# Kernel optimization log

Measured on AMD Instinct MI355X. Metric: run time of the kernel, lower is better.

Reference implementation:

```python
import jax, jax.numpy as jnp
import numpy as np

N_WIN = 8      # windows per side (j = i = n_win)
NUM_HEADS = 8
TOPK = 4


def setup_inputs() -> dict:
    key = jax.random.key(0)
    k1, k2 = jax.random.split(key)
    cv_feature = jax.random.normal(k1, (1, 128, 128, 256), dtype=jnp.float32)
    mv_feature = jax.random.normal(k2, (1, 4, 128, 128, 256), dtype=jnp.float32)
    return {"cv_feature": cv_feature, "mv_feature": mv_feature}


def reference(cv_feature, mv_feature):
    n, H, W, C = cv_feature.shape
    v = mv_feature.shape[1]
    j = i = N_WIN
    h, w = H // j, W // i
    p2, w2 = j * i, h * w
    m = NUM_HEADS
    ch = C // m
    scale = C ** (-0.5)  # module uses d_model**-0.5 for both routing and pixel attn

    # window partition: n (j h)(i w) c -> n (j i) h w c
    cv_patch = cv_feature.reshape(n, j, h, i, w, C).transpose(0, 1, 3, 2, 4, 5).reshape(n, p2, h, w, C)
    mv_patch = mv_feature.reshape(n, v, j, h, i, w, C).transpose(0, 1, 2, 4, 3, 5, 6).reshape(n, v, p2, h, w, C)

    q_pix = cv_patch.reshape(n, p2, w2, C)          # n p2 w2 c
    kv_pix = mv_patch.reshape(n, v, p2, w2, C)      # n v p2 w2 c

    # window-level pooled queries/keys (routing is detached in the original)
    q_win = jax.lax.stop_gradient(cv_patch.mean((2, 3)))            # n p2 c
    k_win = jax.lax.stop_gradient(mv_patch.mean((3, 4)))            # n v p2 c
    k_win = k_win.reshape(n, v * p2, C)

    logits = jnp.einsum('npc,nqc->npq', q_win * scale, k_win)       # n p2 (v p2)
    topk_logit, r_idx = jax.lax.top_k(logits, TOPK)                 # n p2 k
    r_weight = jax.nn.softmax(topk_logit, axis=-1)                  # computed, unused (faithful)

    # gather routed KV windows: n p2 k w2 c
    kv_flat = kv_pix.reshape(n, v * p2, w2, C)
    kv_sel = jnp.take_along_axis(kv_flat[:, None], r_idx[:, :, :, None, None], axis=2)

    # split heads
    k_sel = kv_sel.reshape(n, p2, TOPK, w2, m, ch)                  # n p2 k w2 m ch
    q = q_pix.reshape(n, p2, w2, m, ch)                             # n p2 w2 m ch

    attn = jnp.einsum('npqmc,npkwmc->npmqkw', q * scale, k_sel)
    attn = attn.reshape(n, p2, m, w2, TOPK * w2)
    attn = jax.nn.softmax(attn, axis=-1)

    v_sel = k_sel.transpose(0, 1, 4, 2, 3, 5).reshape(n, p2, m, TOPK * w2, ch)
    out = jnp.einsum('npmqt,npmtc->npmqc', attn, v_sel)             # n p2 m w2 ch

    # merge heads + window un-partition: -> n H W C
    out = out.transpose(0, 1, 3, 2, 4).reshape(n, j, i, h, w, C)
    out = out.transpose(0, 1, 3, 2, 4, 5).reshape(n, H, W, C)
    return out
```

## Files before the change

### kernel.cpp

```cpp
#include <hip/hip_runtime.h>
#include <hip/hip_bf16.h>


typedef __attribute__((ext_vector_type(4))) float f32x4;
typedef __attribute__((ext_vector_type(8))) short s16x8;
typedef __attribute__((ext_vector_type(2))) unsigned u32x2;
typedef __attribute__((ext_vector_type(4))) unsigned u32x4;

#define SCALE 0.0625f
#define LOG2E 1.44269504088896340736f

__device__ inline unsigned cvt_pk_bf16(float lo, float hi) {
  unsigned r;
  asm("v_cvt_pk_bf16_f32 %0, %1, %2" : "=v"(r) : "v"(lo), "v"(hi));
  return r;
}
__device__ inline unsigned pk_bf16_rne(float lo, float hi) {
  unsigned a = __float_as_uint(lo);
  unsigned b = __float_as_uint(hi);
  a += 0x7FFFu + ((a >> 16) & 1u);
  b += 0x7FFFu + ((b >> 16) & 1u);
  return (a >> 16) | (b & 0xFFFF0000u);
}
#if __has_builtin(__builtin_amdgcn_exp2f)
#define EXP2(x) __builtin_amdgcn_exp2f(x)
#else
#define EXP2(x) exp2f(x)
#endif

__global__ __launch_bounds__(256) void k_means(const float* __restrict__ cv,
                                               const float* __restrict__ mv,
                                               float* __restrict__ qwin,
                                               float* __restrict__ kwin) {
  __shared__ f32x4 sm[8][32];
  int wi = blockIdx.x >> 1, half = blockIdx.x & 1;
  int c4 = threadIdx.x & 31, pq = threadIdx.x >> 5;
  const float* base;
  float* dst;
  if (wi < 64) {
    base = cv + ((size_t)((wi >> 3) * 16) * 128 + (wi & 7) * 16) * 256;
    dst = qwin + wi * 256;
  } else {
    int r = wi - 64;
    base = mv + (size_t)(r >> 6) * (128 * 128 * 256)
         + ((size_t)(((r >> 3) & 7) * 16) * 128 + (r & 7) * 16) * 256;
    dst = kwin + r * 256;
  }
  base += half * 128 + c4 * 4;
  f32x4 acc = {0.f, 0.f, 0.f, 0.f};
#pragma unroll 4
  for (int k = 0; k < 32; ++k) {
    int px = pq * 32 + k;
    f32x4 d = *reinterpret_cast<const f32x4*>(base + ((px >> 4) * 128 + (px & 15)) * 256);
    acc += d;
  }
  sm[pq][c4] = acc;
  __syncthreads();
  if (pq == 0) {
    f32x4 s = sm[0][c4];
#pragma unroll
    for (int j = 1; j < 8; ++j) s += sm[j][c4];
    s *= (1.f / 256.f);
    *reinterpret_cast<f32x4*>(dst + half * 128 + c4 * 4) = s;
  }
}

__global__ __launch_bounds__(1024) void k_route(const float* __restrict__ qwin,
                                                const float* __restrict__ kwin,
                                                int* __restrict__ ridx) {
  __shared__ float qrow[256];
  __shared__ float part[4][256];
  __shared__ float sv[256];
  __shared__ float wbv[4];
  __shared__ int wbi[4];
  int p = blockIdx.x, t = threadIdx.x;
  int r = t & 255, cq = t >> 8;
  if (t < 256) qrow[t] = qwin[p * 256 + t] * SCALE;
  __syncthreads();
  const f32x4* kr = reinterpret_cast<const f32x4*>(kwin + r * 256 + cq * 64);
  const float* qr = qrow + cq * 64;
  float dot = 0.f;
#pragma unroll
  for (int i = 0; i < 16; ++i) {
    f32x4 kv = kr[i];
    dot += qr[i * 4 + 0] * kv[0] + qr[i * 4 + 1] * kv[1]
         + qr[i * 4 + 2] * kv[2] + qr[i * 4 + 3] * kv[3];
  }
  part[cq][r] = dot;
  __syncthreads();
  if (t < 256) sv[t] = (part[0][t] + part[1][t]) + (part[2][t] + part[3][t]);
  __syncthreads();
  for (int k = 0; k < 4; ++k) {
    if (t < 256) {
      float v = sv[t];
      int ii = t;
#pragma unroll
      for (int off = 32; off > 0; off >>= 1) {
        float ov = __shfl_down(v, off, 64);
        int oi = __shfl_down(ii, off, 64);
        if (ov > v || (ov == v && oi < ii)) { v = ov; ii = oi; }
      }
      if ((t & 63) == 0) { wbv[t >> 6] = v; wbi[t >> 6] = ii; }
    }
    __syncthreads();
    if (t == 0) {
      float bv = wbv[0]; int bi = wbi[0];
      for (int j = 1; j < 4; ++j)
        if (wbv[j] > bv || (wbv[j] == bv && wbi[j] < bi)) { bv = wbv[j]; bi = wbi[j]; }
      ridx[p * 4 + k] = bi;
      sv[bi] = -3.0e38f;
    }
    __syncthreads();
  }
}

__global__ __launch_bounds__(256, 2) void k_attn(const float* __restrict__ cv,
                                                 const float* __restrict__ mv,
                                                 const int* __restrict__ ridx,
                                                 float* __restrict__ out) {
  __shared__ __align__(16) short kv_lds[256 * 32];

  const int tid = threadIdx.x;
  const int lane = tid & 63, wv = tid >> 6;
  const int g = lane >> 4, c16 = lane & 15;
  const int p = blockIdx.x >> 3, m = blockIdx.x & 7;
  const int py = p >> 3, px = p & 7;

  const int4 ridx4 = *reinterpret_cast<const int4*>(ridx + p * 4);

  const float qs = SCALE * LOG2E;
  s16x8 qf[4];
#pragma unroll
  for (int qt = 0; qt < 4; ++qt) {
    const float* qp = cv + ((size_t)((py * 16 + wv * 4 + qt) * 128) + px * 16 + c16) * 256
                         + m * 32 + g * 8;
    f32x4 a = *reinterpret_cast<const f32x4*>(qp);
    f32x4 b = *reinterpret_cast<const f32x4*>(qp + 4);
    union { u32x4 u; s16x8 s; } cu;
    cu.u[0] = cvt_pk_bf16(a[0] * qs, a[1] * qs);
    cu.u[1] = cvt_pk_bf16(a[2] * qs, a[3] * qs);
    cu.u[2] = cvt_pk_bf16(b[0] * qs, b[1] * qs);
    cu.u[3] = cvt_pk_bf16(b[2] * qs, b[3] * qs);
    qf[qt] = cu.s;
  }

  f32x4 accO[4][2];
  float lsum[4];
#pragma unroll
  for (int qt = 0; qt < 4; ++qt) {
    lsum[qt] = 0.f;
    accO[qt][0] = f32x4{0.f, 0.f, 0.f, 0.f};
    accO[qt][1] = f32x4{0.f, 0.f, 0.f, 0.f};
  }
  const f32x4 zf = {0.f, 0.f, 0.f, 0.f};

  for (int w = 0; w < 4; ++w) {
    if (w) __syncthreads();
    {
      int r = (&ridx4.x)[w];
      const float* srcb = mv + (size_t)(r >> 6) * (128 * 128 * 256)
                        + ((size_t)(((r >> 3) & 7) * 16) * 128 + (r & 7) * 16) * 256 + m * 32;
#pragma unroll
      for (int i = 0; i < 8; ++i) {
        int u = i * 256 + tid;
        int pxl = u >> 3, quad = u & 7;
        f32x4 d = *reinterpret_cast<const f32x4*>(
            srcb + ((pxl >> 4) * 128 + (pxl & 15)) * 256 + quad * 4);
        u32x2 pk;
        pk[0] = cvt_pk_bf16(d[0], d[1]);
        pk[1] = cvt_pk_bf16(d[2], d[3]);
        int off = (pxl >> 2) * 128 + (quad >> 2) * 64 + (pxl & 3) * 16 + (quad & 3) * 4;
        *reinterpret_cast<u32x2*>(&kv_lds[off]) = pk;
      }
    }
    __syncthreads();

#pragma unroll 2
    for (int s = 0; s < 8; ++s) {
      int kr0 = s * 32 + c16;
      int kr1 = kr0 + 16;
      const s16x8 kf0 = *reinterpret_cast<const s16x8*>(
          &kv_lds[(kr0 >> 2) * 128 + (g >> 1) * 64 + (kr0 & 3) * 16 + (g & 1) * 8]);
      const s16x8 kf1 = *reinterpret_cast<const s16x8*>(
          &kv_lds[(kr1 >> 2) * 128 + (g >> 1) * 64 + (kr1 & 3) * 16 + (g & 1) * 8]);
      s16x8 V0, V1;
#pragma unroll
      for (int j = 0; j < 8; ++j) {
        int a = (s * 8 + (j >> 2) * 4 + g) * 128 + (j & 3) * 16 + c16;
        V0[j] = kv_lds[a];
        V1[j] = kv_lds[a + 64];
      }
#pragma unroll
      for (int qt = 0; qt < 4; ++qt) {
        f32x4 sx = __builtin_amdgcn_mfma_f32_16x16x32_bf16(kf0, qf[qt], zf, 0, 0, 0);
        f32x4 sy = __builtin_amdgcn_mfma_f32_16x16x32_bf16(kf1, qf[qt], zf, 0, 0, 0);
        float x0 = EXP2(sx[0]), x1 = EXP2(sx[1]), x2 = EXP2(sx[2]), x3 = EXP2(sx[3]);
        float y0 = EXP2(sy[0]), y1 = EXP2(sy[1]), y2 = EXP2(sy[2]), y3 = EXP2(sy[3]);
        lsum[qt] += ((x0 + x1) + (x2 + x3)) + ((y0 + y1) + (y2 + y3));
        union { u32x4 u; s16x8 s; } pb;
        pb.u[0] = pk_bf16_rne(x0, x1);
        pb.u[1] = pk_bf16_rne(x2, x3);
        pb.u[2] = pk_bf16_rne(y0, y1);
        pb.u[3] = pk_bf16_rne(y2, y3);
        accO[qt][0] = __builtin_amdgcn_mfma_f32_16x16x32_bf16(V0, pb.s, accO[qt][0], 0, 0, 0);
        accO[qt][1] = __builtin_amdgcn_mfma_f32_16x16x32_bf16(V1, pb.s, accO[qt][1], 0, 0, 0);
      }
    }
  }

#pragma unroll
  for (int qt = 0; qt < 4; ++qt) {
    float l = lsum[qt];
    l += __shfl_xor(l, 16, 64);
    l += __shfl_xor(l, 32, 64);
    float rl = 1.f / l;
#pragma unroll
    for (int mt = 0; mt < 2; ++mt) {
      f32x4 o = accO[qt][mt];
      o[0] *= rl; o[1] *= rl; o[2] *= rl; o[3] *= rl;
      float* op = out + ((size_t)((py * 16 + wv * 4 + qt) * 128) + px * 16 + c16) * 256
                      + m * 32 + mt * 16 + g * 4;
      *reinterpret_cast<f32x4*>(op) = o;
    }
  }
}

extern "C" void kernel_launch(void* const* d_in, const int* in_sizes, int n_in,
                              void* d_out, int out_size, void* d_ws, size_t ws_size,
                              hipStream_t stream) {
  const float* cv = (const float*)d_in[0];
  const float* mv = (const float*)d_in[1];
  float* out = (float*)d_out;

  float* qwin = (float*)d_ws;
  float* kwin = qwin + 64 * 256;
  int* ridx = (int*)(kwin + 256 * 256);

  k_means<<<640, 256, 0, stream>>>(cv, mv, qwin, kwin);
  k_route<<<64, 1024, 0, stream>>>(qwin, kwin, ridx);
  k_attn<<<512, 256, 0, stream>>>(cv, mv, ridx, out);
}
```

Before: 71.16 us.

## Fuse window routing top-k into attention kernel, dropping separate route launch

The routing kernel (window logits and top-4 selection) is removed. Each attention block now recomputes the routing for its query window inside its own prologue, reusing the LDS buffer as scratch. This removes one kernel launch and the ridx round trip through global memory. In exchange, the routing work is repeated 8 times per window (once per head block), and each thread reads a full 1 KB kwin row with fewer threads, which lengthens the attention kernel's prologue.

```diff
diff --git a/kernel.cpp b/kernel.cpp
--- a/kernel.cpp
+++ b/kernel.cpp
@@ -65,60 +65,15 @@
   }
 }
 
-__global__ __launch_bounds__(1024) void k_route(const float* __restrict__ qwin,
-                                                const float* __restrict__ kwin,
-                                                int* __restrict__ ridx) {
-  __shared__ float qrow[256];
-  __shared__ float part[4][256];
-  __shared__ float sv[256];
+__global__ __launch_bounds__(256, 2) void k_attn(const float* __restrict__ cv,
+                                                 const float* __restrict__ mv,
+                                                 const float* __restrict__ qwin,
+                                                 const float* __restrict__ kwin,
+                                                 float* __restrict__ out) {
+  __shared__ __align__(16) short kv_lds[256 * 32];
   __shared__ float wbv[4];
   __shared__ int wbi[4];
-  int p = blockIdx.x, t = threadIdx.x;
-  int r = t & 255, cq = t >> 8;
-  if (t < 256) qrow[t] = qwin[p * 256 + t] * SCALE;
-  __syncthreads();
-  const f32x4* kr = reinterpret_cast<const f32x4*>(kwin + r * 256 + cq * 64);
-  const float* qr = qrow + cq * 64;
-  float dot = 0.f;
-#pragma unroll
-  for (int i = 0; i < 16; ++i) {
-    f32x4 kv = kr[i];
-    dot += qr[i * 4 + 0] * kv[0] + qr[i * 4 + 1] * kv[1]
-         + qr[i * 4 + 2] * kv[2] + qr[i * 4 + 3] * kv[3];
-  }
-  part[cq][r] = dot;
-  __syncthreads();
-  if (t < 256) sv[t] = (part[0][t] + part[1][t]) + (part[2][t] + part[3][t]);
-  __syncthreads();
-  for (int k = 0; k < 4; ++k) {
-    if (t < 256) {
-      float v = sv[t];
-      int ii = t;
-#pragma unroll
-      for (int off = 32; off > 0; off >>= 1) {
-        float ov = __shfl_down(v, off, 64);
-        int oi = __shfl_down(ii, off, 64);
-        if (ov > v || (ov == v && oi < ii)) { v = ov; ii = oi; }
-      }
-      if ((t & 63) == 0) { wbv[t >> 6] = v; wbi[t >> 6] = ii; }
-    }
-    __syncthreads();
-    if (t == 0) {
-      float bv = wbv[0]; int bi = wbi[0];
-      for (int j = 1; j < 4; ++j)
-        if (wbv[j] > bv || (wbv[j] == bv && wbi[j] < bi)) { bv = wbv[j]; bi = wbi[j]; }
-      ridx[p * 4 + k] = bi;
-      sv[bi] = -3.0e38f;
-    }
-    __syncthreads();
-  }
-}
-
-__global__ __launch_bounds__(256, 2) void k_attn(const float* __restrict__ cv,
-                                                 const float* __restrict__ mv,
-                                                 const int* __restrict__ ridx,
-                                                 float* __restrict__ out) {
-  __shared__ __align__(16) short kv_lds[256 * 32];
+  __shared__ int rwin4[4];
 
   const int tid = threadIdx.x;
   const int lane = tid & 63, wv = tid >> 6;
@@ -126,7 +81,42 @@
   const int p = blockIdx.x >> 3, m = blockIdx.x & 7;
   const int py = p >> 3, px = p & 7;
 
-  const int4 ridx4 = *reinterpret_cast<const int4*>(ridx + p * 4);
+  {
+    float* qrow = reinterpret_cast<float*>(kv_lds);
+    float* sv = qrow + 256;
+    qrow[tid] = qwin[p * 256 + tid] * SCALE;
+    __syncthreads();
+    const f32x4* kr = reinterpret_cast<const f32x4*>(kwin + tid * 256);
+    float dot = 0.f;
+#pragma unroll 4
+    for (int c4 = 0; c4 < 64; ++c4) {
+      f32x4 kv = kr[c4];
+      dot += qrow[c4 * 4 + 0] * kv[0] + qrow[c4 * 4 + 1] * kv[1]
+           + qrow[c4 * 4 + 2] * kv[2] + qrow[c4 * 4 + 3] * kv[3];
+    }
+    sv[tid] = dot;
+    __syncthreads();
+    for (int k = 0; k < 4; ++k) {
+      float v = sv[tid];
+      int ii = tid;
+#pragma unroll
+      for (int off = 32; off > 0; off >>= 1) {
+        float ov = __shfl_down(v, off, 64);
+        int oi = __shfl_down(ii, off, 64);
+        if (ov > v || (ov == v && oi < ii)) { v = ov; ii = oi; }
+      }
+      if (lane == 0) { wbv[wv] = v; wbi[wv] = ii; }
+      __syncthreads();
+      if (tid == 0) {
+        float bv = wbv[0]; int bi = wbi[0];
+        for (int j = 1; j < 4; ++j)
+          if (wbv[j] > bv || (wbv[j] == bv && wbi[j] < bi)) { bv = wbv[j]; bi = wbi[j]; }
+        rwin4[k] = bi;
+        sv[bi] = -3.0e38f;
+      }
+      __syncthreads();
+    }
+  }
 
   const float qs = SCALE * LOG2E;
   s16x8 qf[4];
@@ -157,7 +147,7 @@
   for (int w = 0; w < 4; ++w) {
     if (w) __syncthreads();
     {
-      int r = (&ridx4.x)[w];
+      int r = rwin4[w];
       const float* srcb = mv + (size_t)(r >> 6) * (128 * 128 * 256)
                         + ((size_t)(((r >> 3) & 7) * 16) * 128 + (r & 7) * 16) * 256 + m * 32;
 #pragma unroll
@@ -234,9 +224,7 @@
 
   float* qwin = (float*)d_ws;
   float* kwin = qwin + 64 * 256;
-  int* ridx = (int*)(kwin + 256 * 256);
 
   k_means<<<640, 256, 0, stream>>>(cv, mv, qwin, kwin);
-  k_route<<<64, 1024, 0, stream>>>(qwin, kwin, ridx);
-  k_attn<<<512, 256, 0, stream>>>(cv, mv, ridx, out);
-}
+  k_attn<<<512, 256, 0, stream>>>(cv, mv, qwin, kwin, out);
+}
```

After: 75.51 us. 6.1% more time.
